# Performance work log

Measured on AMD Instinct MI355X. Metric: run time of the kernel, lower is better.

The kernel has to match this reference:

```python
import jax, jax.numpy as jnp
import numpy as np

UNITS = 512
N_CLASSES = 10
N_FEAT = 3
R_ON = 0.05      # open ratio of the phased-LSTM time gate
ALPHA = 0.001    # leak rate when gate is closed


def setup_inputs() -> dict:
    key = jax.random.key(0)
    ks = jax.random.split(key, 16)
    B, T, F, U, C = 512, 1024, N_FEAT, UNITS, N_CLASSES
    inputs = jax.random.normal(ks[0], (B, T, F), dtype=jnp.float32)
    # irregular, monotonically increasing observation times
    gaps = jax.random.uniform(ks[1], (B, T), dtype=jnp.float32, minval=0.01, maxval=1.0)
    times = jnp.cumsum(gaps, axis=1)
    sc_in = 1.0 / np.sqrt(F)
    sc_u = 1.0 / np.sqrt(U)
    params = {
        'W0': jax.random.normal(ks[2], (F, 4 * U), jnp.float32) * sc_in,
        'U0': jax.random.normal(ks[3], (U, 4 * U), jnp.float32) * sc_u,
        'b0': jnp.zeros((4 * U,), jnp.float32),
        'tau0': jnp.exp(jax.random.uniform(ks[4], (U,), jnp.float32, np.log(10.0), np.log(1000.0))),
        's0': jax.random.uniform(ks[5], (U,), jnp.float32, 0.0, 100.0),
        'W1': jax.random.normal(ks[6], (U, 4 * U), jnp.float32) * sc_u,
        'U1': jax.random.normal(ks[7], (U, 4 * U), jnp.float32) * sc_u,
        'b1': jnp.zeros((4 * U,), jnp.float32),
        'tau1': jnp.exp(jax.random.uniform(ks[8], (U,), jnp.float32, np.log(10.0), np.log(1000.0))),
        's1': jax.random.uniform(ks[9], (U,), jnp.float32, 0.0, 100.0),
        'Wfc': jax.random.normal(ks[10], (U, C), jnp.float32) * sc_u,
        'bfc': jnp.zeros((C,), jnp.float32),
    }
    return dict(inputs=inputs, times=times, **params)


def _plstm_cell(x, t, h, c, W, U, b, tau, s):
    # x:[B,in], t:[B], h,c:[B,U]; standard LSTM gates + phased time gate
    z = x @ W + h @ U + b                     # [B,4U]
    i, f, g, o = jnp.split(z, 4, axis=-1)
    i = jax.nn.sigmoid(i)
    f = jax.nn.sigmoid(f)
    g = jnp.tanh(g)
    o = jax.nn.sigmoid(o)
    c_cand = f * c + i * g
    h_cand = o * jnp.tanh(c_cand)
    # time gate: phase of each unit's oscillation at time t
    phi = jnp.mod(t[:, None] - s, tau) / tau  # [B,U] in [0,1)
    k = jnp.where(phi < 0.5 * R_ON, 2.0 * phi / R_ON,
        jnp.where(phi < R_ON, 2.0 - 2.0 * phi / R_ON, ALPHA * phi))
    c_new = k * c_cand + (1.0 - k) * c
    h_new = k * h_cand + (1.0 - k) * h
    return h_new, c_new


def reference(inputs, times, W0, U0, b0, tau0, s0, W1, U1, b1, tau1, s1, Wfc, bfc):
    B = inputs.shape[0]
    Uh = W0.shape[1] // 4
    h0 = jnp.zeros((B, Uh), inputs.dtype)
    init = (h0, h0, h0, h0)  # (h0, c0, h1, c1)

    def step(carry, xt):
        h_0, c_0, h_1, c_1 = carry
        x, t = xt
        h_0, c_0 = _plstm_cell(x, t, h_0, c_0, W0, U0, b0, tau0, s0)
        h_1, c_1 = _plstm_cell(h_0, t, h_1, c_1, W1, U1, b1, tau1, s1)
        y = jax.nn.softmax(h_1 @ Wfc + bfc, axis=-1)
        return (h_0, c_0, h_1, c_1), y

    xs = (jnp.swapaxes(inputs, 0, 1), jnp.swapaxes(times, 0, 1))  # time-major
    _, preds = jax.lax.scan(step, init, xs)   # [T,B,C]
    return jnp.transpose(preds, (1, 0, 2))     # [B,T,C]
```

## Files before the change

### kernel.cpp

```cpp
#include <hip/hip_runtime.h>
#include <hip/hip_bf16.h>
#include <math.h>

#define TDIM 1024
#define UDIM 512
#define NG   2048
#define NBLK 208

typedef __attribute__((ext_vector_type(8))) short short8;
typedef __attribute__((ext_vector_type(4))) float float4v;

#define OFF_U0T   ((size_t)0)
#define SZ_U0T    ((size_t)NG*UDIM*2)
#define OFF_W1U1T (OFF_U0T + SZ_U0T)
#define SZ_W1U1T  ((size_t)NG*1024*2)
#define OFF_W0P   (OFF_W1U1T + SZ_W1U1T)
#define SZ_W0P    ((size_t)3*NG*4)
#define OFF_B0P   (OFF_W0P + SZ_W0P)
#define OFF_B1P   (OFF_B0P + (size_t)NG*4)
#define OFF_STATE (OFF_B1P + (size_t)NG*4)
#define SZ_HB     ((size_t)512*UDIM*2)
#define SZ_HF     ((size_t)512*UDIM*4)
#define OFF_H0B   (OFF_STATE)
#define OFF_H1B   (OFF_H0B + 4*SZ_HB)
#define OFF_H1F   (OFF_H1B + 4*SZ_HB)
#define OFF_CNT   (OFF_H1F + 4*SZ_HF)
#define STATE_BYTES (8*SZ_HB + 4*SZ_HF + 4096)

#define HSLOT ((size_t)512*UDIM)
#define FSLOT ((size_t)512*UDIM)


__device__ __forceinline__ float rcpf(float x) { return __builtin_amdgcn_rcpf(x); }
__device__ __forceinline__ float sigm(float x) { return rcpf(1.0f + __expf(-x)); }
__device__ __forceinline__ float tanhfast(float x) { return 1.0f - 2.0f * rcpf(1.0f + __expf(2.0f * x)); }

__device__ __forceinline__ void gload16(const void* g, void* l) {
    __builtin_amdgcn_global_load_lds(
        (const __attribute__((address_space(1))) void*)g,
        (__attribute__((address_space(3))) void*)l, 16, 0, 17);
}

__device__ __forceinline__ void store_u16_llc(void* p, unsigned short v) {
    asm volatile("global_store_short %0, %1, off sc0 sc1" :: "v"(p), "v"(v) : "memory");
}
__device__ __forceinline__ void store_f32_llc(void* p, float v) {
    asm volatile("global_store_dword %0, %1, off sc0 sc1" :: "v"(p), "v"(v) : "memory");
}
__device__ __forceinline__ void store_cnt(unsigned* p, unsigned v) {
    asm volatile("global_store_dword %0, %1, off sc0 sc1" :: "v"(p), "v"(v) : "memory");
}

__device__ __forceinline__ int minv(const unsigned* base, int lanemask) {
    unsigned u = __hip_atomic_load(base + (threadIdx.x & lanemask),
                                   __ATOMIC_RELAXED, __HIP_MEMORY_SCOPE_AGENT);
    int x = (int)u;
#pragma unroll
    for (int m = 32; m; m >>= 1) x = min(x, __shfl_xor(x, m, 64));
    return x;
}
__device__ __forceinline__ void wait_min(const unsigned* base, int lanemask,
                                         int tgt, int& seen) {
    while (seen < tgt) {
        seen = minv(base, lanemask);
        if (seen < tgt) __builtin_amdgcn_s_sleep(2);
    }
}
__device__ __forceinline__ void wait_val(unsigned* p, int tgt, int& seen) {
    while (seen < tgt) {
        seen = (int)__hip_atomic_load(p, __ATOMIC_RELAXED, __HIP_MEMORY_SCOPE_AGENT);
        if (seen < tgt) __builtin_amdgcn_s_sleep(2);
    }
}

__device__ __forceinline__ void cell_update(float zi, float zf, float zg, float zo,
                                            float tt, float tvi, float sv,
                                            float& cp, float& hp)
{
    float ig = sigm(zi), fg = sigm(zf), gg = tanhfast(zg), og = sigm(zo);
    float cc = fg * cp + ig * gg;
    float hc = og * tanhfast(cc);
    float q  = (tt - sv) * tvi;
    float ph = q - floorf(q);
    float kg = (ph < 0.025f) ? (ph * 40.0f)
             : (ph < 0.05f ? 2.0f - ph * 40.0f : 0.001f * ph);
    cp = kg * cc + (1.0f - kg) * cp;
    hp = kg * hc + (1.0f - kg) * hp;
}

__global__ void prep_kernel(const float* __restrict__ W0, const float* __restrict__ U0,
                            const float* __restrict__ b0, const float* __restrict__ W1,
                            const float* __restrict__ U1, const float* __restrict__ b1,
                            char* __restrict__ ws)
{
    int idx = blockIdx.x * 256 + threadIdx.x;
    int n = idx >> 10;
    int k = idx & 1023;
    int oc = (n & 3) * UDIM + (n >> 2);
    __hip_bfloat16* U0t = (__hip_bfloat16*)(ws + OFF_U0T);
    __hip_bfloat16* Wc  = (__hip_bfloat16*)(ws + OFF_W1U1T);
    float* W0p = (float*)(ws + OFF_W0P);
    float* b0p = (float*)(ws + OFF_B0P);
    float* b1p = (float*)(ws + OFF_B1P);
    if (k < 512) U0t[(size_t)n * 512 + k] = __float2bfloat16(U0[(size_t)k * NG + oc]);
    float wv = (k < 512) ? W1[(size_t)k * NG + oc] : U1[(size_t)(k - 512) * NG + oc];
    Wc[(size_t)n * 1024 + k] = __float2bfloat16(wv);
    if (k < 3) W0p[k * NG + n] = W0[(size_t)k * NG + oc];
    if (k == 0) { b0p[n] = b0[oc]; b1p[n] = b1[oc]; }
}

__device__ void layer0_persist(char* smem, int blk,
    const float* __restrict__ inputs, const float* __restrict__ times,
    const float* __restrict__ tau0, const float* __restrict__ s0v, char* __restrict__ ws)
{
    const int msl = blk >> 4, nsl = blk & 15;
    unsigned* cnt = (unsigned*)(ws + OFF_CNT);
    const unsigned* P0G = cnt + msl * 16;
    const unsigned* P1G = cnt + 64 + msl * 32;
    unsigned* myP0 = cnt + msl * 16 + nsl;
    int rawSeen = 0, warSeen = 0;
    const int tid = threadIdx.x;
    const int wave = tid >> 6, lane = tid & 63, lr = lane & 15, lq = lane >> 4;
    const int mg = wave >> 2, nw = wave & 3;
    const int colbase = nsl * 128 + nw * 32;

    const __hip_bfloat16* U0t = (const __hip_bfloat16*)(ws + OFF_U0T);
    const float* b0p = (const float*)(ws + OFF_B0P);
    const float* W0p = (const float*)(ws + OFF_W0P);
    __hip_bfloat16* h0b = (__hip_bfloat16*)(ws + OFF_H0B);

    short8 Bf[32];
#pragma unroll
    for (int i = 0; i < 16; ++i) {
        int l = (nsl + i) & 15;
        Bf[i]      = *(const short8*)(U0t + (size_t)(colbase + lr) * 512 + l * 32 + lq * 8);
        Bf[16 + i] = *(const short8*)(U0t + (size_t)(colbase + 16 + lr) * 512 + l * 32 + lq * 8);
    }

    const int cu = tid & 31, crb = tid >> 5;
    const int uu = nsl * 32 + cu;
    const int pcc = nsl * 128 + cu * 4;
    const float4v bias4 = *(const float4v*)(b0p + pcc);
    const float4v w0x = *(const float4v*)(W0p + pcc);
    const float4v w0y = *(const float4v*)(W0p + NG + pcc);
    const float4v w0z = *(const float4v*)(W0p + 2 * NG + pcc);
    const float tvi = 1.0f / tau0[uu], sv = s0v[uu];

    float c0r[8], h0r[8];
#pragma unroll
    for (int i = 0; i < 8; ++i) { c0r[i] = 0.0f; h0r[i] = 0.0f; }

    const int g_row = tid >> 2;
    const int g_q   = (tid & 3) ^ ((g_row >> 1) & 3);

    for (int s = 0; s < TDIM; ++s) {
        if (s >= 4) wait_min(P1G, 31, s - 3, warSeen);
        wait_min(P0G, 15, s, rawSeen);

        const __hip_bfloat16* Arow = h0b + ((size_t)((s + 3) & 3)) * HSLOT +
            (size_t)(msl * 128 + g_row) * 512 + g_q * 8;
        __hip_bfloat16* h0w = h0b + ((size_t)(s & 3)) * HSLOT;
#pragma unroll
        for (int j = 0; j < 6; ++j)
            gload16(Arow + ((nsl + j) & 15) * 32, smem + j * 8192 + wave * 1024);

        const float4v z4 = {0.0f, 0.0f, 0.0f, 0.0f};
        float4v acc[4][2];
#pragma unroll
        for (int mf = 0; mf < 4; ++mf) { acc[mf][0] = z4; acc[mf][1] = z4; }

#pragma unroll
        for (int I = 0; I < 8; ++I) {
            asm volatile("s_waitcnt vmcnt(%0)" :: "i"((I <= 5) ? 4 : (14 - 2 * I)) : "memory");
            __builtin_amdgcn_s_barrier();
            __builtin_amdgcn_sched_barrier(0);
            if (I < 5) {
                int t0 = 2 * I + 6, t1 = 2 * I + 7;
                gload16(Arow + ((nsl + t0) & 15) * 32, smem + (t0 & 7) * 8192 + wave * 1024);
                gload16(Arow + ((nsl + t1) & 15) * 32, smem + (t1 & 7) * 8192 + wave * 1024);
            }
            const short* sA0 = (const short*)(smem + ((2 * I) & 7) * 8192);
            const short* sA1 = (const short*)(smem + ((2 * I + 1) & 7) * 8192);
            short8 aF0[4], aF1[4];
#pragma unroll
            for (int mf = 0; mf < 4; ++mf) {
                int row = mg * 64 + mf * 16 + lr;
                int q = lq ^ ((row >> 1) & 3);
                aF0[mf] = *(const short8*)(sA0 + row * 32 + q * 8);
                aF1[mf] = *(const short8*)(sA1 + row * 32 + q * 8);
            }
#pragma unroll
            for (int mf = 0; mf < 4; ++mf) {
                acc[mf][0] = __builtin_amdgcn_mfma_f32_16x16x32_bf16(aF0[mf], Bf[2 * I],          acc[mf][0], 0, 0, 0);
                acc[mf][1] = __builtin_amdgcn_mfma_f32_16x16x32_bf16(aF0[mf], Bf[16 + 2 * I],     acc[mf][1], 0, 0, 0);
                acc[mf][0] = __builtin_amdgcn_mfma_f32_16x16x32_bf16(aF1[mf], Bf[2 * I + 1],      acc[mf][0], 0, 0, 0);
                acc[mf][1] = __builtin_amdgcn_mfma_f32_16x16x32_bf16(aF1[mf], Bf[16 + 2 * I + 1], acc[mf][1], 0, 0, 0);
            }
        }
        __syncthreads();
        float* Z = (float*)smem;
#pragma unroll
        for (int pass = 0; pass < 2; ++pass) {
            if (mg == pass) {
#pragma unroll
                for (int mf = 0; mf < 4; ++mf)
#pragma unroll
                    for (int nf = 0; nf < 2; ++nf)
#pragma unroll
                        for (int i = 0; i < 4; ++i)
                            Z[(mf * 16 + lq * 4 + i) * 132 + nw * 32 + nf * 16 + lr] = acc[mf][nf][i];
            }
            __syncthreads();
#pragma unroll
            for (int cc = 0; cc < 4; ++cc) {
                int rl = crb + 16 * cc;
                int b = msl * 128 + pass * 64 + rl;
                float4v z = *(const float4v*)(Z + rl * 132 + cu * 4);
                const float* xp = inputs + ((size_t)b * TDIM + s) * 3;
                float x0 = xp[0], x1 = xp[1], x2 = xp[2];
                float zi = z[0] + bias4[0] + x0 * w0x[0] + x1 * w0y[0] + x2 * w0z[0];
                float zf = z[1] + bias4[1] + x0 * w0x[1] + x1 * w0y[1] + x2 * w0z[1];
                float zg = z[2] + bias4[2] + x0 * w0x[2] + x1 * w0y[2] + x2 * w0z[2];
                float zo = z[3] + bias4[3] + x0 * w0x[3] + x1 * w0y[3] + x2 * w0z[3];
                float tt = times[(size_t)b * TDIM + s];
                cell_update(zi, zf, zg, zo, tt, tvi, sv, c0r[pass * 4 + cc], h0r[pass * 4 + cc]);
                __hip_bfloat16 hb = __float2bfloat16(h0r[pass * 4 + cc]);
                store_u16_llc(h0w + (size_t)b * 512 + uu, *(unsigned short*)&hb);
            }
            __syncthreads();
        }
        if (tid == 0) store_cnt(myP0, (unsigned)(s + 1));
    }
}

__device__ void layer1_persist(char* smem, int blk,
    const float* __restrict__ times,
    const float* __restrict__ tau1, const float* __restrict__ s1v, char* __restrict__ ws)
{
    const int m8 = blk >> 4, nsl = blk & 15;
    const int grp = m8 >> 1, half = m8 & 1;
    unsigned* cnt = (unsigned*)(ws + OFF_CNT);
    const unsigned* P0G = cnt + grp * 16;
    const unsigned* P1R = cnt + 64 + grp * 32 + half * 16;
    unsigned* myP1 = cnt + 64 + grp * 32 + half * 16 + nsl;
    unsigned* PF = cnt + 192 + grp * 16;
    int raw0Seen = 0, raw1Seen = 0, pfSeen = 0;
    const int tid = threadIdx.x;
    const int wave = tid >> 6, lane = tid & 63, lr = lane & 15, lq = lane >> 4;
    const int kg = wave >> 2, nw = wave & 3;
    const int colbase = nsl * 128 + nw * 32;
    const int r1 = nsl & 7;

    const __hip_bfloat16* Wc = (const __hip_bfloat16*)(ws + OFF_W1U1T);
    const float* b1p = (const float*)(ws + OFF_B1P);
    __hip_bfloat16* h0b = (__hip_bfloat16*)(ws + OFF_H0B);
    __hip_bfloat16* h1b = (__hip_bfloat16*)(ws + OFF_H1B);
    float* h1f = (float*)(ws + OFF_H1F);

    short8 Bf[32];
#pragma unroll
    for (int i = 0; i < 8; ++i) {
        int l = (i + r1) & 7;
#pragma unroll
        for (int kk = 0; kk < 2; ++kk) {
            Bf[i * 2 + kk]      = *(const short8*)(Wc + (size_t)(colbase + lr) * 1024 + kg * 512 + (l * 2 + kk) * 32 + lq * 8);
            Bf[16 + i * 2 + kk] = *(const short8*)(Wc + (size_t)(colbase + 16 + lr) * 1024 + kg * 512 + (l * 2 + kk) * 32 + lq * 8);
        }
    }

    const int cu = tid & 31, crb = tid >> 5;
    const int uu = nsl * 32 + cu;
    const int pcc = nsl * 128 + cu * 4;
    const float4v bias4 = *(const float4v*)(b1p + pcc);
    const float tvi = 1.0f / tau1[uu], sv = s1v[uu];

    float c1r[4], h1r[4];
#pragma unroll
    for (int i = 0; i < 4; ++i) { c1r[i] = 0.0f; h1r[i] = 0.0f; }

    const int g_row = tid >> 3;
    const int g_q   = (tid & 7) ^ (g_row & 7);

    for (int s = 1; s <= TDIM; ++s) {
        const int t = s - 1;
        if (s >= 5) wait_val(PF, 4 * (s - 4), pfSeen);
        wait_min(P0G, 15, s, raw0Seen);
        wait_min(P1R, 15, s - 1, raw1Seen);

        const __hip_bfloat16* A0 = h0b + ((size_t)((s + 3) & 3)) * HSLOT +
            (size_t)(m8 * 64 + g_row) * 512 + g_q * 8;
        const __hip_bfloat16* A1 = h1b + ((size_t)((s + 2) & 3)) * HSLOT +
            (size_t)(m8 * 64 + g_row) * 512 + g_q * 8;
        __hip_bfloat16* h1w = h1b + ((size_t)((s + 3) & 3)) * HSLOT;
        float* h1fw = h1f + ((size_t)((s + 3) & 3)) * FSLOT;
#pragma unroll
        for (int J = 0; J < 3; ++J) {
            int l = (J + r1) & 7;
            gload16(A0 + l * 64, smem + (J & 3) * 8192 + wave * 1024);
            gload16(A1 + l * 64, smem + 32768 + (J & 3) * 8192 + wave * 1024);
        }
        const float4v z4 = {0.0f, 0.0f, 0.0f, 0.0f};
        float4v acc[4][2];
#pragma unroll
        for (int mf = 0; mf < 4; ++mf) { acc[mf][0] = z4; acc[mf][1] = z4; }

#pragma unroll
        for (int J = 0; J < 8; ++J) {
            asm volatile("s_waitcnt vmcnt(%0)" :: "i"((J + 2 < 8) ? 4 : ((7 - J) * 2)) : "memory");
            __builtin_amdgcn_s_barrier();
            __builtin_amdgcn_sched_barrier(0);
            if (J + 3 < 8) {
                int l = (J + 3 + r1) & 7;
                gload16(A0 + l * 64, smem + ((J + 3) & 3) * 8192 + wave * 1024);
                gload16(A1 + l * 64, smem + 32768 + ((J + 3) & 3) * 8192 + wave * 1024);
            }
            const short* sA = (const short*)(smem + kg * 32768 + (J & 3) * 8192);
#pragma unroll
            for (int kk = 0; kk < 2; ++kk) {
                short8 aF[4];
#pragma unroll
                for (int mf = 0; mf < 4; ++mf) {
                    int row = mf * 16 + lr;
                    int q = (kk * 4 + lq) ^ (row & 7);
                    aF[mf] = *(const short8*)(sA + row * 64 + q * 8);
                }
#pragma unroll
                for (int mf = 0; mf < 4; ++mf) {
                    acc[mf][0] = __builtin_amdgcn_mfma_f32_16x16x32_bf16(aF[mf], Bf[J * 2 + kk],      acc[mf][0], 0, 0, 0);
                    acc[mf][1] = __builtin_amdgcn_mfma_f32_16x16x32_bf16(aF[mf], Bf[16 + J * 2 + kk], acc[mf][1], 0, 0, 0);
                }
            }
        }
        __syncthreads();
        float* Z = (float*)smem;
        if (kg == 1) {
#pragma unroll
            for (int mf = 0; mf < 4; ++mf)
#pragma unroll
                for (int nf = 0; nf < 2; ++nf)
#pragma unroll
                    for (int i = 0; i < 4; ++i)
                        Z[(mf * 16 + lq * 4 + i) * 132 + nw * 32 + nf * 16 + lr] = acc[mf][nf][i];
        }
        __syncthreads();
        if (kg == 0) {
#pragma unroll
            for (int mf = 0; mf < 4; ++mf)
#pragma unroll
                for (int nf = 0; nf < 2; ++nf)
#pragma unroll
                    for (int i = 0; i < 4; ++i) {
                        int idx = (mf * 16 + lq * 4 + i) * 132 + nw * 32 + nf * 16 + lr;
                        Z[idx] += acc[mf][nf][i];
                    }
        }
        __syncthreads();
#pragma unroll
        for (int cc = 0; cc < 4; ++cc) {
            int rl = crb + 16 * cc;
            int b = m8 * 64 + rl;
            float4v z = *(const float4v*)(Z + rl * 132 + cu * 4);
            float zi = z[0] + bias4[0];
            float zf = z[1] + bias4[1];
            float zg = z[2] + bias4[2];
            float zo = z[3] + bias4[3];
            float tt = times[(size_t)b * TDIM + t];
            cell_update(zi, zf, zg, zo, tt, tvi, sv, c1r[cc], h1r[cc]);
            __hip_bfloat16 hb = __float2bfloat16(h1r[cc]);
            store_u16_llc(h1w + (size_t)b * 512 + uu, *(unsigned short*)&hb);
            store_f32_llc(h1fw + (size_t)b * 512 + uu, h1r[cc]);
        }
        __syncthreads();
        if (tid == 0) store_cnt(myP1, (unsigned)s);
    }
}

__device__ void fc_persist(char* smem, int blk, const float* __restrict__ Wfc,
                           const float* __restrict__ bfc,
                           char* __restrict__ ws, float* __restrict__ out)
{
    const int grp = blk >> 2;
    unsigned* cnt = (unsigned*)(ws + OFF_CNT);
    const unsigned* P1R = cnt + 64 + grp * 32 + ((blk >> 1) & 1) * 16;
    unsigned* PF = cnt + 192 + grp * 16;
    int raw1Seen = 0;
    const int tid = threadIdx.x, wave = tid >> 6, lane = tid & 63;
    const float* h1f = (const float*)(ws + OFF_H1F);
    const int rbase = blk * 32;

    for (int s = 2; s <= TDIM + 1; ++s) {
        int t = s - 2;
        wait_min(P1R, 15, s - 1, raw1Seen);
        const char* h = (const char*)(h1f + ((size_t)((s + 2) & 3)) * FSLOT +
                                      (size_t)rbase * 512);
#pragma unroll
        for (int k = 0; k < 8; ++k)
            gload16(h + ((size_t)(tid + k * 512)) * 16, smem + k * 8192 + wave * 1024);
        asm volatile("s_waitcnt vmcnt(0)" ::: "memory");
        __syncthreads();
        if (tid == 0)
            __hip_atomic_fetch_add(PF, 1u, __ATOMIC_RELAXED, __HIP_MEMORY_SCOPE_AGENT);
        const float* hl = (const float*)smem;
        for (int ri = 0; ri < 4; ++ri) {
            int rl = wave * 4 + ri;
            int row = rbase + rl;
            float a[10];
#pragma unroll
            for (int c = 0; c < 10; ++c) a[c] = 0.0f;
#pragma unroll
            for (int itr = 0; itr < 8; ++itr) {
                float hv = hl[(size_t)rl * 512 + itr * 64 + lane];
                const float* wp = &Wfc[(size_t)(itr * 64 + lane) * 10];
#pragma unroll
                for (int c = 0; c < 10; ++c) a[c] += hv * wp[c];
            }
#pragma unroll
            for (int c = 0; c < 10; ++c)
                for (int m = 32; m; m >>= 1) a[c] += __shfl_xor(a[c], m, 64);
            if (lane == 0) {
                float mx = -1e30f;
#pragma unroll
                for (int c = 0; c < 10; ++c) { a[c] += bfc[c]; mx = fmaxf(mx, a[c]); }
                float sum = 0.0f;
#pragma unroll
                for (int c = 0; c < 10; ++c) { a[c] = __expf(a[c] - mx); sum += a[c]; }
                float inv = 1.0f / sum;
                float* op = &out[((size_t)row * TDIM + t) * 10];
#pragma unroll
                for (int c = 0; c < 10; ++c) op[c] = a[c] * inv;
            }
        }
        __syncthreads();
    }
}

__global__ __launch_bounds__(512, 2)
void persist_kernel(const float* __restrict__ inputs, const float* __restrict__ times,
                    const float* __restrict__ tau0, const float* __restrict__ s0v,
                    const float* __restrict__ tau1, const float* __restrict__ s1v,
                    const float* __restrict__ Wfc, const float* __restrict__ bfc,
                    char* __restrict__ ws, float* __restrict__ out)
{
    __shared__ __align__(16) char smem[65536];
    int blk = blockIdx.x;
    if (blk < 64)       layer0_persist(smem, blk, inputs, times, tau0, s0v, ws);
    else if (blk < 192) layer1_persist(smem, blk - 64, times, tau1, s1v, ws);
    else                fc_persist(smem, blk - 192, Wfc, bfc, ws, out);
}

extern "C" void kernel_launch(void* const* d_in, const int* in_sizes, int n_in,
                              void* d_out, int out_size, void* d_ws, size_t ws_size,
                              hipStream_t stream) {
    const float* inputs = (const float*)d_in[0];
    const float* times  = (const float*)d_in[1];
    const float* W0   = (const float*)d_in[2];
    const float* U0   = (const float*)d_in[3];
    const float* b0   = (const float*)d_in[4];
    const float* tau0 = (const float*)d_in[5];
    const float* s0   = (const float*)d_in[6];
    const float* W1   = (const float*)d_in[7];
    const float* U1   = (const float*)d_in[8];
    const float* b1   = (const float*)d_in[9];
    const float* tau1 = (const float*)d_in[10];
    const float* s1   = (const float*)d_in[11];
    const float* Wfc  = (const float*)d_in[12];
    const float* bfc  = (const float*)d_in[13];
    float* out = (float*)d_out;
    char* ws = (char*)d_ws;

    hipMemsetAsync(ws + OFF_STATE, 0, STATE_BYTES, stream);
    prep_kernel<<<(NG * 1024) / 256, 256, 0, stream>>>(W0, U0, b0, W1, U1, b1, ws);

    void* kargs[] = {(void*)&inputs, (void*)&times, (void*)&tau0, (void*)&s0,
                     (void*)&tau1, (void*)&s1, (void*)&Wfc, (void*)&bfc,
                     (void*)&ws, (void*)&out};
    hipLaunchCooperativeKernel((const void*)persist_kernel, dim3(NBLK), dim3(512),
                               kargs, 0, stream);
}
```

Before: 12.34 ms.

## Replace all-producer barrier waits with per-slice readiness checks before each load

Instead of waiting until every producer block in a group has published step s before starting the recurrent GEMM, each wave polls the per-producer counters and, before each K-slice load, waits only for the producer that owns that slice. This lets consumption of early slices overlap with producers still finishing later slices, cutting the lockstep stall on the cross-block dependency. Layer 0's epilogue also moves from two 64-row passes with extra barriers to one 128-row pass, which needs more shared memory (raised to 69632 bytes). The risks are extra polling and shuffle overhead inside the load pipeline, and possible occupancy or correctness issues with the larger shared buffer and the finer-grained ordering.

```diff
diff --git a/kernel.cpp b/kernel.cpp
--- a/kernel.cpp
+++ b/kernel.cpp
@@ -51,18 +51,23 @@
     asm volatile("global_store_dword %0, %1, off sc0 sc1" :: "v"(p), "v"(v) : "memory");
 }
 
-__device__ __forceinline__ int minv(const unsigned* base, int lanemask) {
-    unsigned u = __hip_atomic_load(base + (threadIdx.x & lanemask),
-                                   __ATOMIC_RELAXED, __HIP_MEMORY_SCOPE_AGENT);
-    int x = (int)u;
-#pragma unroll
-    for (int m = 32; m; m >>= 1) x = min(x, __shfl_xor(x, m, 64));
-    return x;
+__device__ __forceinline__ int pollv16(const unsigned* base) {
+    return (int)__hip_atomic_load(base + (threadIdx.x & 15),
+                                  __ATOMIC_RELAXED, __HIP_MEMORY_SCOPE_AGENT);
+}
+__device__ __forceinline__ int pollv2(const unsigned* a, const unsigned* b) {
+    const unsigned* p = ((threadIdx.x & 32) ? b : a) + (threadIdx.x & 15);
+    return (int)__hip_atomic_load(p, __ATOMIC_RELAXED, __HIP_MEMORY_SCOPE_AGENT);
 }
 __device__ __forceinline__ void wait_min(const unsigned* base, int lanemask,
                                          int tgt, int& seen) {
     while (seen < tgt) {
-        seen = minv(base, lanemask);
+        unsigned u = __hip_atomic_load(base + (threadIdx.x & lanemask),
+                                       __ATOMIC_RELAXED, __HIP_MEMORY_SCOPE_AGENT);
+        int x = (int)u;
+#pragma unroll
+        for (int m = 32; m; m >>= 1) x = min(x, __shfl_xor(x, m, 64));
+        seen = x;
         if (seen < tgt) __builtin_amdgcn_s_sleep(2);
     }
 }
@@ -118,7 +123,7 @@
     const unsigned* P0G = cnt + msl * 16;
     const unsigned* P1G = cnt + 64 + msl * 32;
     unsigned* myP0 = cnt + msl * 16 + nsl;
-    int rawSeen = 0, warSeen = 0;
+    int seenv = 0, warSeen = 0;
     const int tid = threadIdx.x;
     const int wave = tid >> 6, lane = tid & 63, lr = lane & 15, lq = lane >> 4;
     const int mg = wave >> 2, nw = wave & 3;
@@ -155,14 +160,26 @@
 
     for (int s = 0; s < TDIM; ++s) {
         if (s >= 4) wait_min(P1G, 31, s - 3, warSeen);
-        wait_min(P0G, 15, s, rawSeen);
+        {
+            int x = seenv;
+#pragma unroll
+            for (int m = 32; m; m >>= 1) x = min(x, __shfl_xor(x, m, 64));
+            if (x < s) seenv = pollv16(P0G);
+        }
 
         const __hip_bfloat16* Arow = h0b + ((size_t)((s + 3) & 3)) * HSLOT +
             (size_t)(msl * 128 + g_row) * 512 + g_q * 8;
         __hip_bfloat16* h0w = h0b + ((size_t)(s & 3)) * HSLOT;
 #pragma unroll
-        for (int j = 0; j < 6; ++j)
-            gload16(Arow + ((nsl + j) & 15) * 32, smem + j * 8192 + wave * 1024);
+        for (int j = 0; j < 6; ++j) {
+            int l = (nsl + j) & 15;
+            if (j)
+                while (__shfl(seenv, l, 64) < s) {
+                    __builtin_amdgcn_s_sleep(1);
+                    seenv = pollv16(P0G);
+                }
+            gload16(Arow + l * 32, smem + j * 8192 + wave * 1024);
+        }
 
         const float4v z4 = {0.0f, 0.0f, 0.0f, 0.0f};
         float4v acc[4][2];
@@ -176,8 +193,17 @@
             __builtin_amdgcn_sched_barrier(0);
             if (I < 5) {
                 int t0 = 2 * I + 6, t1 = 2 * I + 7;
-                gload16(Arow + ((nsl + t0) & 15) * 32, smem + (t0 & 7) * 8192 + wave * 1024);
-                gload16(Arow + ((nsl + t1) & 15) * 32, smem + (t1 & 7) * 8192 + wave * 1024);
+                int l0 = (nsl + t0) & 15, l1 = (nsl + t1) & 15;
+                while (__shfl(seenv, l0, 64) < s) {
+                    __builtin_amdgcn_s_sleep(1);
+                    seenv = pollv16(P0G);
+                }
+                while (__shfl(seenv, l1, 64) < s) {
+                    __builtin_amdgcn_s_sleep(1);
+                    seenv = pollv16(P0G);
+                }
+                gload16(Arow + l0 * 32, smem + (t0 & 7) * 8192 + wave * 1024);
+                gload16(Arow + l1 * 32, smem + (t1 & 7) * 8192 + wave * 1024);
             }
             const short* sA0 = (const short*)(smem + ((2 * I) & 7) * 8192);
             const short* sA1 = (const short*)(smem + ((2 * I + 1) & 7) * 8192);
@@ -200,35 +226,30 @@
         __syncthreads();
         float* Z = (float*)smem;
 #pragma unroll
-        for (int pass = 0; pass < 2; ++pass) {
-            if (mg == pass) {
-#pragma unroll
-                for (int mf = 0; mf < 4; ++mf)
-#pragma unroll
-                    for (int nf = 0; nf < 2; ++nf)
-#pragma unroll
-                        for (int i = 0; i < 4; ++i)
-                            Z[(mf * 16 + lq * 4 + i) * 132 + nw * 32 + nf * 16 + lr] = acc[mf][nf][i];
-            }
-            __syncthreads();
-#pragma unroll
-            for (int cc = 0; cc < 4; ++cc) {
-                int rl = crb + 16 * cc;
-                int b = msl * 128 + pass * 64 + rl;
-                float4v z = *(const float4v*)(Z + rl * 132 + cu * 4);
-                const float* xp = inputs + ((size_t)b * TDIM + s) * 3;
-                float x0 = xp[0], x1 = xp[1], x2 = xp[2];
-                float zi = z[0] + bias4[0] + x0 * w0x[0] + x1 * w0y[0] + x2 * w0z[0];
-                float zf = z[1] + bias4[1] + x0 * w0x[1] + x1 * w0y[1] + x2 * w0z[1];
-                float zg = z[2] + bias4[2] + x0 * w0x[2] + x1 * w0y[2] + x2 * w0z[2];
-                float zo = z[3] + bias4[3] + x0 * w0x[3] + x1 * w0y[3] + x2 * w0z[3];
-                float tt = times[(size_t)b * TDIM + s];
-                cell_update(zi, zf, zg, zo, tt, tvi, sv, c0r[pass * 4 + cc], h0r[pass * 4 + cc]);
-                __hip_bfloat16 hb = __float2bfloat16(h0r[pass * 4 + cc]);
-                store_u16_llc(h0w + (size_t)b * 512 + uu, *(unsigned short*)&hb);
-            }
-            __syncthreads();
-        }
+        for (int mf = 0; mf < 4; ++mf)
+#pragma unroll
+            for (int nf = 0; nf < 2; ++nf)
+#pragma unroll
+                for (int i = 0; i < 4; ++i)
+                    Z[(mg * 64 + mf * 16 + lq * 4 + i) * 132 + nw * 32 + nf * 16 + lr] = acc[mf][nf][i];
+        __syncthreads();
+#pragma unroll
+        for (int cc = 0; cc < 8; ++cc) {
+            int rl = crb + 16 * cc;
+            int b = msl * 128 + rl;
+            float4v z = *(const float4v*)(Z + rl * 132 + cu * 4);
+            const float* xp = inputs + ((size_t)b * TDIM + s) * 3;
+            float x0 = xp[0], x1 = xp[1], x2 = xp[2];
+            float zi = z[0] + bias4[0] + x0 * w0x[0] + x1 * w0y[0] + x2 * w0z[0];
+            float zf = z[1] + bias4[1] + x0 * w0x[1] + x1 * w0y[1] + x2 * w0z[1];
+            float zg = z[2] + bias4[2] + x0 * w0x[2] + x1 * w0y[2] + x2 * w0z[2];
+            float zo = z[3] + bias4[3] + x0 * w0x[3] + x1 * w0y[3] + x2 * w0z[3];
+            float tt = times[(size_t)b * TDIM + s];
+            cell_update(zi, zf, zg, zo, tt, tvi, sv, c0r[cc], h0r[cc]);
+            __hip_bfloat16 hb = __float2bfloat16(h0r[cc]);
+            store_u16_llc(h0w + (size_t)b * 512 + uu, *(unsigned short*)&hb);
+        }
+        __syncthreads();
         if (tid == 0) store_cnt(myP0, (unsigned)(s + 1));
     }
 }
@@ -244,7 +265,7 @@
     const unsigned* P1R = cnt + 64 + grp * 32 + half * 16;
     unsigned* myP1 = cnt + 64 + grp * 32 + half * 16 + nsl;
     unsigned* PF = cnt + 192 + grp * 16;
-    int raw0Seen = 0, raw1Seen = 0, pfSeen = 0;
+    int sv2 = 0, pfSeen = 0;
     const int tid = threadIdx.x;
     const int wave = tid >> 6, lane = tid & 63, lr = lane & 15, lq = lane >> 4;
     const int kg = wave >> 2, nw = wave & 3;
@@ -272,7 +293,7 @@
     const int uu = nsl * 32 + cu;
     const int pcc = nsl * 128 + cu * 4;
     const float4v bias4 = *(const float4v*)(b1p + pcc);
-    const float tvi = 1.0f / tau1[uu], sv = s1v[uu];
+    const float tvi = 1.0f / tau1[uu], svv = s1v[uu];
 
     float c1r[4], h1r[4];
 #pragma unroll
@@ -284,8 +305,13 @@
     for (int s = 1; s <= TDIM; ++s) {
         const int t = s - 1;
         if (s >= 5) wait_val(PF, 4 * (s - 4), pfSeen);
-        wait_min(P0G, 15, s, raw0Seen);
-        wait_min(P1R, 15, s - 1, raw1Seen);
+        {
+            int x = sv2;
+#pragma unroll
+            for (int m = 16; m; m >>= 1) x = min(x, __shfl_xor(x, m, 64));
+            bool need = (lane < 32) ? (x < s) : (x < s - 1);
+            if (__any(need)) sv2 = pollv2(P0G, P1R);
+        }
 
         const __hip_bfloat16* A0 = h0b + ((size_t)((s + 3) & 3)) * HSLOT +
             (size_t)(m8 * 64 + g_row) * 512 + g_q * 8;
@@ -296,6 +322,12 @@
 #pragma unroll
         for (int J = 0; J < 3; ++J) {
             int l = (J + r1) & 7;
+            while (min(__shfl(sv2, 2 * l, 64), __shfl(sv2, 2 * l + 1, 64)) < s) {
+                __builtin_amdgcn_s_sleep(1); sv2 = pollv2(P0G, P1R);
+            }
+            while (min(__shfl(sv2, 32 + 2 * l, 64), __shfl(sv2, 32 + 2 * l + 1, 64)) < s - 1) {
+                __builtin_amdgcn_s_sleep(1); sv2 = pollv2(P0G, P1R);
+            }
             gload16(A0 + l * 64, smem + (J & 3) * 8192 + wave * 1024);
             gload16(A1 + l * 64, smem + 32768 + (J & 3) * 8192 + wave * 1024);
         }
@@ -311,6 +343,12 @@
             __builtin_amdgcn_sched_barrier(0);
             if (J + 3 < 8) {
                 int l = (J + 3 + r1) & 7;
+                while (min(__shfl(sv2, 2 * l, 64), __shfl(sv2, 2 * l + 1, 64)) < s) {
+                    __builtin_amdgcn_s_sleep(1); sv2 = pollv2(P0G, P1R);
+                }
+                while (min(__shfl(sv2, 32 + 2 * l, 64), __shfl(sv2, 32 + 2 * l + 1, 64)) < s - 1) {
+                    __builtin_amdgcn_s_sleep(1); sv2 = pollv2(P0G, P1R);
+                }
                 gload16(A0 + l * 64, smem + ((J + 3) & 3) * 8192 + wave * 1024);
                 gload16(A1 + l * 64, smem + 32768 + ((J + 3) & 3) * 8192 + wave * 1024);
             }
@@ -365,7 +403,7 @@
             float zg = z[2] + bias4[2];
             float zo = z[3] + bias4[3];
             float tt = times[(size_t)b * TDIM + t];
-            cell_update(zi, zf, zg, zo, tt, tvi, sv, c1r[cc], h1r[cc]);
+            cell_update(zi, zf, zg, zo, tt, tvi, svv, c1r[cc], h1r[cc]);
             __hip_bfloat16 hb = __float2bfloat16(h1r[cc]);
             store_u16_llc(h1w + (size_t)b * 512 + uu, *(unsigned short*)&hb);
             store_f32_llc(h1fw + (size_t)b * 512 + uu, h1r[cc]);
@@ -441,7 +479,7 @@
                     const float* __restrict__ Wfc, const float* __restrict__ bfc,
                     char* __restrict__ ws, float* __restrict__ out)
 {
-    __shared__ __align__(16) char smem[65536];
+    __shared__ __align__(16) char smem[69632];
     int blk = blockIdx.x;
     if (blk < 64)       layer0_persist(smem, blk, inputs, times, tau0, s0v, ws);
     else if (blk < 192) layer1_persist(smem, blk - 64, times, tau1, s1v, ws);
```

Result: slower. 17.22 ms (+39.6%).
